# Performance work log

Hardware: AMD Instinct MI355X
Metric: run time of the kernel (lower is better)

Reference implementation:

```python
import jax, jax.numpy as jnp
import numpy as np

sigmoid = jax.nn.sigmoid

def lstm_layer(x_seq, W, U, b, act):
    """Keras-style LSTM. x_seq: [B,T,D], W: [D,4H], U: [H,4H], b: [4H].
    Gate order i,f,c,o. recurrent_activation=sigmoid, cell/output activation=act.
    Returns full hidden sequence [B,T,H]."""
    B, T, D = x_seq.shape
    H = U.shape[0]
    # precompute input contribution for all timesteps: [T,B,4H]
    xW = jnp.einsum('btd,dg->tbg', x_seq, W) + b
    h0 = jnp.zeros((B, H), x_seq.dtype)
    c0 = jnp.zeros((B, H), x_seq.dtype)

    def step(carry, xw_t):
        h, c = carry
        z = xw_t + h @ U  # [B,4H]
        i, f, g, o = jnp.split(z, 4, axis=-1)
        i = sigmoid(i)
        f = sigmoid(f)
        g = act(g)
        o = sigmoid(o)
        c_new = f * c + i * g
        h_new = o * act(c_new)
        return (h_new, c_new), h_new

    (_, _), hs = jax.lax.scan(step, (h0, c0), xW)  # hs: [T,B,H]
    return jnp.transpose(hs, (1, 0, 2))


def setup_inputs() -> dict:
    key = jax.random.key(0)
    ks = jax.random.split(key, 7)
    B, T, V, E, H1, H2 = 4096, 200, 30000, 32, 32, 1
    x = jax.random.randint(ks[0], (B, T), 0, V, dtype=jnp.int32)
    emb = jax.random.normal(ks[1], (V, E), jnp.float32) * 0.05
    W1 = jax.random.normal(ks[2], (E, 4 * H1), jnp.float32) * 0.1
    U1 = jax.random.normal(ks[3], (H1, 4 * H1), jnp.float32) * 0.1
    b1 = jnp.zeros((4 * H1,), jnp.float32)
    W2 = jax.random.normal(ks[4], (H1, 4 * H2), jnp.float32) * 0.1
    U2 = jax.random.normal(ks[5], (H2, 4 * H2), jnp.float32) * 0.1
    b2 = jnp.zeros((4 * H2,), jnp.float32)
    return {"x": x, "emb": emb, "W1": W1, "U1": U1, "b1": b1,
            "W2": W2, "U2": U2, "b2": b2}


def reference(x, emb, W1, U1, b1, W2, U2, b2):
    e = emb[x]                                   # [B,T,32] embedding lookup
    h1 = lstm_layer(e, W1, U1, b1, jnp.tanh)     # [B,T,32]
    h2 = lstm_layer(h1, W2, U2, b2, sigmoid)     # [B,T,1] (activation='sigmoid')
    return h2[:, -1, :]                          # return_sequences=False -> last step [B,1]
```

## Files before the change

### kernel.cpp

```cpp
#include <hip/hip_runtime.h>
#include <hip/hip_bf16.h>

#define DEV_INLINE __device__ __forceinline__

typedef float v2f __attribute__((ext_vector_type(2)));
typedef __fp16 h2v __attribute__((ext_vector_type(2)));

DEV_INLINE float rlf(float v, int l) {
    return __uint_as_float(__builtin_amdgcn_readlane(__float_as_uint(v), l));
}
DEV_INLINE int rfl(int v) { return __builtin_amdgcn_readfirstlane(v); }
DEV_INLINE float sigmoid_f(float x) { return __builtin_amdgcn_rcpf(1.0f + __expf(-x)); }

#if __has_builtin(__builtin_amdgcn_fdot2)
DEV_INLINE float fdot2(h2v a, h2v b, float c) { return __builtin_amdgcn_fdot2(a, b, c, false); }
#else
DEV_INLINE float fdot2(h2v a, h2v b, float c) {
    return fmaf((float)a[0], (float)b[0], fmaf((float)a[1], (float)b[1], c));
}
#endif

DEV_INLINE void lds_barrier() {
    asm volatile("s_waitcnt lgkmcnt(0)" ::: "memory");
    __builtin_amdgcn_s_barrier();
    asm volatile("" ::: "memory");
}

template<int N>
DEV_INLINE float ror_add(float v) {
    int r = __builtin_amdgcn_update_dpp(0, __float_as_int(v), 0x120 + N, 0xF, 0xF, true);
    return v + __int_as_float(r);
}

DEV_INLINE void bcast_halves(float v, bool low, float& lo_b, float& hi_b) {
#if __has_builtin(__builtin_amdgcn_permlane32_swap)
    auto r = __builtin_amdgcn_permlane32_swap(__float_as_uint(v), __float_as_uint(v),
                                              false, false);
    lo_b = __uint_as_float(r[0]);
    hi_b = __uint_as_float(r[1]);
#else
    float vx = __shfl_xor(v, 32);
    lo_b = low ? v : vx;
    hi_b = low ? vx : v;
#endif
}

__global__ __launch_bounds__(256) void embw_kernel(
    const float* __restrict__ emb, const float* __restrict__ W1,
    const float* __restrict__ b1, float* __restrict__ embW)
{
    __shared__ float w[4096];
    const int tid = threadIdx.x;
#pragma unroll
    for (int i = 0; i < 16; ++i) w[tid + i * 256] = W1[tid + i * 256];
    __syncthreads();

    const int c   = tid & 127;
    const int sub = tid >> 7;
    const float bc = b1[c];
    const int v0 = blockIdx.x * 16;

#pragma unroll
    for (int r = sub; r < 16; r += 2) {
        const int v = v0 + r;
        const float* e = emb + (size_t)v * 32;
        float acc = bc;
#pragma unroll
        for (int d = 0; d < 32; ++d) acc = fmaf(e[d], w[d * 128 + c], acc);
        embW[(size_t)v * 128 + c] = acc;
    }
}

template<int MODE>
__global__ __launch_bounds__(128, 8) void lstm_kernel(
    const int* __restrict__ x, const float* __restrict__ embW,
    const float* __restrict__ emb, const float* __restrict__ W1,
    const float* __restrict__ b1, const float* __restrict__ U1,
    const float* __restrict__ W2, const float* __restrict__ U2,
    const float* __restrict__ b2, float* __restrict__ out, int T)
{
    const int lane = threadIdx.x & 63;
    const int wv   = threadIdx.x >> 6;
    const int b    = blockIdx.x;
    const bool low = lane < 32;
    const int col  = wv * 64 + lane;

    h2v up[16];
#pragma unroll
    for (int m = 0; m < 16; ++m) {
        h2v t;
        t[0] = (__fp16)U1[(2 * m) * 128 + col];
        t[1] = (__fp16)U1[(2 * m + 1) * 128 + col];
        up[m] = t;
    }

    h2v wp[16]; float bcol = 0.f;
    if constexpr (MODE == 1) {
#pragma unroll
        for (int m = 0; m < 16; ++m) {
            h2v t;
            t[0] = (__fp16)W1[(2 * m) * 128 + col];
            t[1] = (__fp16)W1[(2 * m + 1) * 128 + col];
            wp[m] = t;
        }
        bcol = b1[col];
    }

    const int gsel = lane >> 4;
    const int pm   = lane & 15;
    h2v w2s;
    w2s[0] = (__fp16)W2[(2 * pm) * 4 + gsel];
    w2s[1] = (__fp16)W2[(2 * pm + 1) * 4 + gsel];
    const float u2s = U2[gsel];
    const float b2s = b2[gsel];

    __shared__ v2f gbuf[2][32];
    __shared__ __align__(16) __fp16 hbuf[32];

    const int* xrow = x + b * T;

    float h = 0.f, c = 0.f, h2 = 0.f, c2 = 0.f;
    h2v hp[16];
#pragma unroll
    for (int m = 0; m < 16; ++m) hp[m] = __builtin_bit_cast(h2v, 0);

    int idxA = rfl(xrow[0]);
    int idxB = rfl(xrow[1]);
    int idxC = rfl(xrow[2]);

    float zc = 0.f, zn = 0.f;
    if constexpr (MODE == 0) {
        zc = embW[(size_t)idxA * 128 + col];
        zn = embW[(size_t)idxB * 128 + col];
    }

#pragma unroll 2
    for (int t = 0; t < T; ++t) {
        float zf = 0.f;
        if constexpr (MODE == 0) zf = embW[(size_t)idxC * 128 + col];
        int idxN = rfl(xrow[(t + 3 < T) ? (t + 3) : (T - 1)]);

        float a0, a1 = 0.f, a2 = 0.f, a3 = 0.f;
        if constexpr (MODE == 0) {
            a0 = zc;
        } else {
            a0 = bcol;
            const v2f* e2 = reinterpret_cast<const v2f*>(emb + (size_t)idxA * 32);
#pragma unroll
            for (int m = 0; m < 16; m += 2) {
                v2f ea = e2[m], eb = e2[m + 1];
                a0 = fdot2(__builtin_amdgcn_cvt_pkrtz(ea.x, ea.y), wp[m],     a0);
                a1 = fdot2(__builtin_amdgcn_cvt_pkrtz(eb.x, eb.y), wp[m + 1], a1);
            }
        }
#pragma unroll
        for (int m = 0; m < 16; m += 4) {
            a0 = fdot2(hp[m],     up[m],     a0);
            a1 = fdot2(hp[m + 1], up[m + 1], a1);
            a2 = fdot2(hp[m + 2], up[m + 2], a2);
            a3 = fdot2(hp[m + 3], up[m + 3], a3);
        }
        const float z = (a0 + a1) + (a2 + a3);

        float iv, fv, gv, ov;
        if (wv == 0) {
            float sa = sigmoid_f(z);
            bcast_halves(sa, low, iv, fv);
            if (low) gbuf[0][lane] = (v2f){iv, fv};
        } else {
            float xb = low ? 2.0f * z : z;
            float u  = sigmoid_f(xb);
            float rb = low ? 2.0f * u - 1.0f : u;
            bcast_halves(rb, low, gv, ov);
            if (low) gbuf[1][lane] = (v2f){gv, ov};
        }
        lds_barrier();

        {
            v2f other = gbuf[wv ^ 1][lane & 31];
            if (wv == 0) { gv = other.x; ov = other.y; }
            else         { iv = other.x; fv = other.y; }
        }

        c = fmaf(fv, c, iv * gv);
        float tc = 2.0f * sigmoid_f(2.0f * c) - 1.0f;
        h = ov * tc;

        if (wv == 0 && low) hbuf[lane] = (__fp16)h;
        lds_barrier();

        {
            const int4* hb4 = reinterpret_cast<const int4*>(hbuf);
            int4 q0 = hb4[0], q1 = hb4[1], q2 = hb4[2], q3 = hb4[3];
            hp[0]  = __builtin_bit_cast(h2v, q0.x); hp[1]  = __builtin_bit_cast(h2v, q0.y);
            hp[2]  = __builtin_bit_cast(h2v, q0.z); hp[3]  = __builtin_bit_cast(h2v, q0.w);
            hp[4]  = __builtin_bit_cast(h2v, q1.x); hp[5]  = __builtin_bit_cast(h2v, q1.y);
            hp[6]  = __builtin_bit_cast(h2v, q1.z); hp[7]  = __builtin_bit_cast(h2v, q1.w);
            hp[8]  = __builtin_bit_cast(h2v, q2.x); hp[9]  = __builtin_bit_cast(h2v, q2.y);
            hp[10] = __builtin_bit_cast(h2v, q2.z); hp[11] = __builtin_bit_cast(h2v, q2.w);
            hp[12] = __builtin_bit_cast(h2v, q3.x); hp[13] = __builtin_bit_cast(h2v, q3.y);
            hp[14] = __builtin_bit_cast(h2v, q3.z); hp[15] = __builtin_bit_cast(h2v, q3.w);
        }

        if (wv == 1) {
            const int* hbi = reinterpret_cast<const int*>(hbuf);
            h2v php = __builtin_bit_cast(h2v, hbi[pm]);
            float p = fdot2(php, w2s, 0.f);
            p = ror_add<8>(p);
            p = ror_add<4>(p);
            p = ror_add<2>(p);
            p = ror_add<1>(p);
            float s2 = sigmoid_f(p + fmaf(u2s, h2, b2s));
            float i2 = rlf(s2, 0),  f2 = rlf(s2, 16);
            float g2 = rlf(s2, 32), o2 = rlf(s2, 48);
            c2 = fmaf(f2, c2, i2 * g2);
            h2 = o2 * sigmoid_f(c2);
        }

        zc = zn; zn = zf;
        idxA = idxB; idxB = idxC; idxC = idxN;
    }

    if (wv == 1 && lane == 0) out[b] = h2;
}

extern "C" void kernel_launch(void* const* d_in, const int* in_sizes, int n_in,
                              void* d_out, int out_size, void* d_ws, size_t ws_size,
                              hipStream_t stream) {
    const int*   x   = (const int*)d_in[0];
    const float* emb = (const float*)d_in[1];
    const float* W1  = (const float*)d_in[2];
    const float* U1  = (const float*)d_in[3];
    const float* b1  = (const float*)d_in[4];
    const float* W2  = (const float*)d_in[5];
    const float* U2  = (const float*)d_in[6];
    const float* b2  = (const float*)d_in[7];
    float* out = (float*)d_out;

    const int V = in_sizes[1] / 32;
    const int T = 200;
    const int B = in_sizes[0] / T;

    const size_t need = (size_t)V * 128 * sizeof(float);
    if (ws_size >= need) {
        float* embW = (float*)d_ws;
        embw_kernel<<<V / 16, 256, 0, stream>>>(emb, W1, b1, embW);
        lstm_kernel<0><<<B, 128, 0, stream>>>(x, embW, emb, W1, b1, U1,
                                              W2, U2, b2, out, T);
    } else {
        lstm_kernel<1><<<B, 128, 0, stream>>>(x, nullptr, emb, W1, b1, U1,
                                              W2, U2, b2, out, T);
    }
}
```

Before: 295.7 us.

## Replace precomputed embW table with fp16 embedding rows and in-kernel input projection

Drops the precomputed [V,128] fp32 embedding-times-W1 table. Embeddings are now packed once to fp16 and each step loads the 64-byte row, computing the input projection with packed dot products against register-held W1. The layer-2 update is deferred by one step so it runs after the recurrent matvec, overlapping with layer-1 gate work, and occupancy hint is lowered to 4 blocks. This cuts gather traffic per step (64 bytes vs 512 bytes per token) at the cost of extra fdot2 ALU work and more registers.

```diff
diff --git a/kernel.cpp b/kernel.cpp
--- a/kernel.cpp
+++ b/kernel.cpp
@@ -45,35 +45,29 @@
 #endif
 }
 
-__global__ __launch_bounds__(256) void embw_kernel(
-    const float* __restrict__ emb, const float* __restrict__ W1,
-    const float* __restrict__ b1, float* __restrict__ embW)
+__global__ __launch_bounds__(256) void pack_kernel(
+    const float* __restrict__ emb, __fp16* __restrict__ emb16, int npair)
 {
-    __shared__ float w[4096];
-    const int tid = threadIdx.x;
-#pragma unroll
-    for (int i = 0; i < 16; ++i) w[tid + i * 256] = W1[tid + i * 256];
-    __syncthreads();
-
-    const int c   = tid & 127;
-    const int sub = tid >> 7;
-    const float bc = b1[c];
-    const int v0 = blockIdx.x * 16;
-
-#pragma unroll
-    for (int r = sub; r < 16; r += 2) {
-        const int v = v0 + r;
-        const float* e = emb + (size_t)v * 32;
-        float acc = bc;
-#pragma unroll
-        for (int d = 0; d < 32; ++d) acc = fmaf(e[d], w[d * 128 + c], acc);
-        embW[(size_t)v * 128 + c] = acc;
+    int i = blockIdx.x * 256 + threadIdx.x;
+    if (i < npair) {
+        v2f e = reinterpret_cast<const v2f*>(emb)[i];
+        reinterpret_cast<h2v*>(emb16)[i] = __builtin_amdgcn_cvt_pkrtz(e.x, e.y);
+    }
+}
+
+DEV_INLINE void unpack_row(const int4 (&q)[4], h2v (&ec)[16]) {
+#pragma unroll
+    for (int i = 0; i < 4; ++i) {
+        ec[4 * i + 0] = __builtin_bit_cast(h2v, q[i].x);
+        ec[4 * i + 1] = __builtin_bit_cast(h2v, q[i].y);
+        ec[4 * i + 2] = __builtin_bit_cast(h2v, q[i].z);
+        ec[4 * i + 3] = __builtin_bit_cast(h2v, q[i].w);
     }
 }
 
 template<int MODE>
-__global__ __launch_bounds__(128, 8) void lstm_kernel(
-    const int* __restrict__ x, const float* __restrict__ embW,
+__global__ __launch_bounds__(128, 4) void lstm_kernel(
+    const int* __restrict__ x, const __fp16* __restrict__ emb16,
     const float* __restrict__ emb, const float* __restrict__ W1,
     const float* __restrict__ b1, const float* __restrict__ U1,
     const float* __restrict__ W2, const float* __restrict__ U2,
@@ -85,26 +79,17 @@
     const bool low = lane < 32;
     const int col  = wv * 64 + lane;
 
-    h2v up[16];
+    h2v up[16], wp[16];
 #pragma unroll
     for (int m = 0; m < 16; ++m) {
-        h2v t;
-        t[0] = (__fp16)U1[(2 * m) * 128 + col];
-        t[1] = (__fp16)U1[(2 * m + 1) * 128 + col];
-        up[m] = t;
-    }
-
-    h2v wp[16]; float bcol = 0.f;
-    if constexpr (MODE == 1) {
-#pragma unroll
-        for (int m = 0; m < 16; ++m) {
-            h2v t;
-            t[0] = (__fp16)W1[(2 * m) * 128 + col];
-            t[1] = (__fp16)W1[(2 * m + 1) * 128 + col];
-            wp[m] = t;
-        }
-        bcol = b1[col];
-    }
+        h2v tu, tw;
+        tu[0] = (__fp16)U1[(2 * m) * 128 + col];
+        tu[1] = (__fp16)U1[(2 * m + 1) * 128 + col];
+        tw[0] = (__fp16)W1[(2 * m) * 128 + col];
+        tw[1] = (__fp16)W1[(2 * m + 1) * 128 + col];
+        up[m] = tu; wp[m] = tw;
+    }
+    const float bcol = b1[col];
 
     const int gsel = lane >> 4;
     const int pm   = lane & 15;
@@ -128,30 +113,60 @@
     int idxB = rfl(xrow[1]);
     int idxC = rfl(xrow[2]);
 
-    float zc = 0.f, zn = 0.f;
+#define LAYER2_UPDATE()                                                       \
+    do {                                                                      \
+        const int* hbi = reinterpret_cast<const int*>(hbuf);                  \
+        h2v php = __builtin_bit_cast(h2v, hbi[pm]);                           \
+        float p = fdot2(php, w2s, 0.f);                                       \
+        p = ror_add<8>(p);                                                    \
+        p = ror_add<4>(p);                                                    \
+        p = ror_add<2>(p);                                                    \
+        p = ror_add<1>(p);                             \
+        float s2 = sigmoid_f(p + fmaf(u2s, h2, b2s));    \
+        float i2 = rlf(s2, 0),  f2 = rlf(s2, 16);                             \
+        float g2 = rlf(s2, 32), o2 = rlf(s2, 48);                             \
+        c2 = fmaf(f2, c2, i2 * g2);                                           \
+        h2 = o2 * sigmoid_f(c2);                    \
+    } while (0)
+
+    h2v ec[16];
     if constexpr (MODE == 0) {
-        zc = embW[(size_t)idxA * 128 + col];
-        zn = embW[(size_t)idxB * 128 + col];
+        int4 q[4];
+        const int4* r = reinterpret_cast<const int4*>(emb16 + (size_t)idxA * 32);
+#pragma unroll
+        for (int i = 0; i < 4; ++i) q[i] = r[i];
+        unpack_row(q, ec);
+    } else {
+        const v2f* e2 = reinterpret_cast<const v2f*>(emb + (size_t)idxA * 32);
+#pragma unroll
+        for (int m = 0; m < 16; ++m) {
+            v2f e = e2[m];
+            ec[m] = __builtin_amdgcn_cvt_pkrtz(e.x, e.y);
+        }
     }
 
 #pragma unroll 2
     for (int t = 0; t < T; ++t) {
-        float zf = 0.f;
-        if constexpr (MODE == 0) zf = embW[(size_t)idxC * 128 + col];
+        int4 nq[4];
+        v2f nf[16];
+        if constexpr (MODE == 0) {
+            const int4* r = reinterpret_cast<const int4*>(emb16 + (size_t)idxB * 32);
+#pragma unroll
+            for (int i = 0; i < 4; ++i) nq[i] = r[i];
+        } else {
+            const v2f* e2 = reinterpret_cast<const v2f*>(emb + (size_t)idxB * 32);
+#pragma unroll
+            for (int m = 0; m < 16; ++m) nf[m] = e2[m];
+        }
         int idxN = rfl(xrow[(t + 3 < T) ? (t + 3) : (T - 1)]);
 
-        float a0, a1 = 0.f, a2 = 0.f, a3 = 0.f;
-        if constexpr (MODE == 0) {
-            a0 = zc;
-        } else {
-            a0 = bcol;
-            const v2f* e2 = reinterpret_cast<const v2f*>(emb + (size_t)idxA * 32);
-#pragma unroll
-            for (int m = 0; m < 16; m += 2) {
-                v2f ea = e2[m], eb = e2[m + 1];
-                a0 = fdot2(__builtin_amdgcn_cvt_pkrtz(ea.x, ea.y), wp[m],     a0);
-                a1 = fdot2(__builtin_amdgcn_cvt_pkrtz(eb.x, eb.y), wp[m + 1], a1);
-            }
+        float a0 = bcol, a1 = 0.f, a2 = 0.f, a3 = 0.f;
+#pragma unroll
+        for (int m = 0; m < 16; m += 4) {
+            a0 = fdot2(ec[m],     wp[m],     a0);
+            a1 = fdot2(ec[m + 1], wp[m + 1], a1);
+            a2 = fdot2(ec[m + 2], wp[m + 2], a2);
+            a3 = fdot2(ec[m + 3], wp[m + 3], a3);
         }
 #pragma unroll
         for (int m = 0; m < 16; m += 4) {
@@ -161,6 +176,8 @@
             a3 = fdot2(hp[m + 3], up[m + 3], a3);
         }
         const float z = (a0 + a1) + (a2 + a3);
+
+        if (wv == 1 && t) LAYER2_UPDATE();
 
         float iv, fv, gv, ov;
         if (wv == 0) {
@@ -202,26 +219,19 @@
             hp[14] = __builtin_bit_cast(h2v, q3.z); hp[15] = __builtin_bit_cast(h2v, q3.w);
         }
 
-        if (wv == 1) {
-            const int* hbi = reinterpret_cast<const int*>(hbuf);
-            h2v php = __builtin_bit_cast(h2v, hbi[pm]);
-            float p = fdot2(php, w2s, 0.f);
-            p = ror_add<8>(p);
-            p = ror_add<4>(p);
-            p = ror_add<2>(p);
-            p = ror_add<1>(p);
-            float s2 = sigmoid_f(p + fmaf(u2s, h2, b2s));
-            float i2 = rlf(s2, 0),  f2 = rlf(s2, 16);
-            float g2 = rlf(s2, 32), o2 = rlf(s2, 48);
-            c2 = fmaf(f2, c2, i2 * g2);
-            h2 = o2 * sigmoid_f(c2);
-        }
-
-        zc = zn; zn = zf;
+        if constexpr (MODE == 0) {
+            unpack_row(nq, ec);
+        } else {
+#pragma unroll
+            for (int m = 0; m < 16; ++m) ec[m] = __builtin_amdgcn_cvt_pkrtz(nf[m].x, nf[m].y);
+        }
         idxA = idxB; idxB = idxC; idxC = idxN;
     }
 
+    if (wv == 1) LAYER2_UPDATE();
+
     if (wv == 1 && lane == 0) out[b] = h2;
+#undef LAYER2_UPDATE
 }
 
 extern "C" void kernel_launch(void* const* d_in, const int* in_sizes, int n_in,
@@ -241,11 +251,12 @@
     const int T = 200;
     const int B = in_sizes[0] / T;
 
-    const size_t need = (size_t)V * 128 * sizeof(float);
+    const size_t need = (size_t)V * 32 * sizeof(__fp16);
     if (ws_size >= need) {
-        float* embW = (float*)d_ws;
-        embw_kernel<<<V / 16, 256, 0, stream>>>(emb, W1, b1, embW);
-        lstm_kernel<0><<<B, 128, 0, stream>>>(x, embW, emb, W1, b1, U1,
+        __fp16* emb16 = (__fp16*)d_ws;
+        const int npair = V * 16;
+        pack_kernel<<<(npair + 255) / 256, 256, 0, stream>>>(emb, emb16, npair);
+        lstm_kernel<0><<<B, 128, 0, stream>>>(x, emb16, emb, W1, b1, U1,
                                               W2, U2, b2, out, T);
     } else {
         lstm_kernel<1><<<B, 128, 0, stream>>>(x, nullptr, emb, W1, b1, U1,
```

New measurement: 341.3 us. 1.15x slower.
